# Kernel optimization log

Measured on AMD Instinct MI355X. Metric: run time of the kernel, lower is better.

## Reference

```python
import jax, jax.numpy as jnp
import numpy as np

HIDDEN = 1024
N_EXPERTS = 8
TOP_K = 2
INTER = 1408
N_SHARED = 2
SCALE = 1.0  # routed_scaling_factor


def setup_inputs() -> dict:
    key = jax.random.key(0)
    ks = jax.random.split(key, 9)
    s_h = 1.0 / np.sqrt(HIDDEN)
    s_i = 1.0 / np.sqrt(INTER)
    x = jax.random.normal(ks[0], (2, 2048, HIDDEN), dtype=jnp.float32)
    gate_w = jax.random.uniform(ks[1], (N_EXPERTS, HIDDEN), jnp.float32, -s_h, s_h)  # kaiming_uniform-ish
    # routed experts: SwiGLU (gate, up, down), stacked over experts
    wg = jax.random.uniform(ks[2], (N_EXPERTS, HIDDEN, INTER), jnp.float32, -s_h, s_h)
    wu = jax.random.uniform(ks[3], (N_EXPERTS, HIDDEN, INTER), jnp.float32, -s_h, s_h)
    wd = jax.random.uniform(ks[4], (N_EXPERTS, INTER, HIDDEN), jnp.float32, -s_i, s_i)
    # shared experts: one SwiGLU with intermediate = INTER * N_SHARED
    si = INTER * N_SHARED
    s_si = 1.0 / np.sqrt(si)
    swg = jax.random.uniform(ks[5], (HIDDEN, si), jnp.float32, -s_h, s_h)
    swu = jax.random.uniform(ks[6], (HIDDEN, si), jnp.float32, -s_h, s_h)
    swd = jax.random.uniform(ks[7], (si, HIDDEN), jnp.float32, -s_si, s_si)
    return {"x": x, "gate_w": gate_w, "wg": wg, "wu": wu, "wd": wd,
            "swg": swg, "swu": swu, "swd": swd}


def reference(x, gate_w, wg, wu, wd, swg, swu, swd):
    B, S, H = x.shape
    xf = x.reshape(-1, H)                              # [T, H]
    T = xf.shape[0]
    # --- MoEGate (fp32) ---
    logits = xf.astype(jnp.float32) @ gate_w.astype(jnp.float32).T   # [T, E]
    scores = jax.nn.softmax(logits, axis=-1)
    topw, topi = jax.lax.top_k(scores, TOP_K)          # [T, K]
    denom = topw.sum(axis=-1, keepdims=True) + 1e-20   # norm_topk_prob (top_k > 1)
    topw = topw / denom * SCALE
    # dense combine weights [T, E]: zero except at top-k expert slots
    wdense = jnp.zeros((T, N_EXPERTS), jnp.float32).at[
        jnp.arange(T)[:, None], topi].set(topw)
    # --- routed experts (SwiGLU), computed densely per expert and combined ---
    hg = jnp.einsum('th,ehi->eti', xf, wg)             # [E, T, I]
    hu = jnp.einsum('th,ehi->eti', xf, wu)             # [E, T, I]
    eo = jnp.einsum('eti,eih->eth', jax.nn.silu(hg) * hu, wd)   # [E, T, H]
    y = jnp.einsum('te,eth->th', wdense, eo)           # weighted scatter-combine
    # --- shared experts ---
    shared = (jax.nn.silu(xf @ swg) * (xf @ swu)) @ swd
    return (y + shared).reshape(B, S, H)
```

## Files before the change

kernel.cpp:

```cpp
#include <hip/hip_runtime.h>
#include <hip/hip_bf16.h>
#include <math.h>

#define HIDDEN 1024
#define NEXP 8
#define TOPK 2
#define INTER 1408
#define SINTER 2816
#define NTOK 4096
#define NROWS (NTOK * TOPK)
#define NPANEL 10
#define TROWS 16384
#define MAXT 136

typedef unsigned short ushort_t;
typedef __attribute__((ext_vector_type(8))) short short8;
typedef __attribute__((ext_vector_type(4))) float f32x4;

__device__ __forceinline__ ushort_t f2bf(float f) {
    unsigned int b = __float_as_uint(f);
    unsigned int r = (b + 0x7FFFu + ((b >> 16) & 1u)) >> 16;
    return (ushort_t)r;
}
__device__ __forceinline__ float bf2f(ushort_t u) {
    return __uint_as_float(((unsigned int)u) << 16);
}
__device__ __forceinline__ float silu_f(float g) {
    return g * (1.0f / (1.0f + __expf(-g)));
}
__device__ __forceinline__ int imin(int a, int b) { return a < b ? a : b; }

#define GLDS16(gp, lp) __builtin_amdgcn_global_load_lds(                     \
    (const __attribute__((address_space(1))) void*)(gp),                     \
    (__attribute__((address_space(3))) void*)(lp), 16, 0, 0)

__global__ void conv_x(const float* __restrict__ src, ushort_t* __restrict__ dst) {
    int i = (blockIdx.x * 256 + threadIdx.x) * 4;
    float4 v = *reinterpret_cast<const float4*>(&src[i]);
    union { ushort_t h[4]; unsigned long long ll; } p;
    p.h[0] = f2bf(v.x); p.h[1] = f2bf(v.y); p.h[2] = f2bf(v.z); p.h[3] = f2bf(v.w);
    *reinterpret_cast<unsigned long long*>(&dst[i]) = p.ll;
}

__global__ void tconv(const float* __restrict__ src, ushort_t* __restrict__ dst,
                      int R, int C, long sstride, long dstride) {
    src += (size_t)blockIdx.z * sstride;
    dst += (size_t)blockIdx.z * dstride;
    __shared__ float tile[32][33];
    int ct = blockIdx.x * 32, rt = blockIdx.y * 32;
    int tx = threadIdx.x, ty = threadIdx.y;
#pragma unroll
    for (int i = 0; i < 4; i++)
        tile[ty + 8 * i][tx] = src[(size_t)(rt + ty + 8 * i) * C + ct + tx];
    __syncthreads();
#pragma unroll
    for (int i = 0; i < 4; i++)
        dst[(size_t)(ct + ty + 8 * i) * R + rt + tx] = f2bf(tile[tx][ty + 8 * i]);
}

__global__ void gate_kernel(const float* __restrict__ x, const float* __restrict__ gw,
                            int* __restrict__ top_i, float* __restrict__ top_w) {
    int t = blockIdx.x;
    int lane = threadIdx.x;
    const float* xr = x + (size_t)t * HIDDEN;
    float acc[NEXP];
#pragma unroll
    for (int e = 0; e < NEXP; e++) acc[e] = 0.f;
    for (int j = 0; j < HIDDEN / 64; j++) {
        float xv = xr[lane + 64 * j];
#pragma unroll
        for (int e = 0; e < NEXP; e++)
            acc[e] = fmaf(xv, gw[e * HIDDEN + lane + 64 * j], acc[e]);
    }
#pragma unroll
    for (int e = 0; e < NEXP; e++) {
        float v = acc[e];
        for (int off = 32; off > 0; off >>= 1) v += __shfl_xor(v, off, 64);
        acc[e] = v;
    }
    if (lane == 0) {
        float mx = acc[0];
        for (int e = 1; e < NEXP; e++) mx = fmaxf(mx, acc[e]);
        float s[NEXP];
        float sum = 0.f;
        for (int e = 0; e < NEXP; e++) { s[e] = __expf(acc[e] - mx); sum += s[e]; }
        float inv = 1.0f / sum;
        for (int e = 0; e < NEXP; e++) s[e] *= inv;
        int e0 = 0;
        for (int e = 1; e < NEXP; e++) if (s[e] > s[e0]) e0 = e;
        int e1 = -1;
        for (int e = 0; e < NEXP; e++) {
            if (e == e0) continue;
            if (e1 < 0 || s[e] > s[e1]) e1 = e;
        }
        float w0 = s[e0], w1 = s[e1];
        float denom = w0 + w1 + 1e-20f;
        top_i[t * 2 + 0] = e0;
        top_i[t * 2 + 1] = e1;
        top_w[t * 2 + 0] = w0 / denom;
        top_w[t * 2 + 1] = w1 / denom;
    }
}

__global__ void assign_kernel(const int* __restrict__ top_i, int* __restrict__ cnt,
                              int* __restrict__ rnk) {
    int j = blockIdx.x * blockDim.x + threadIdx.x;
    if (j < NROWS) rnk[j] = atomicAdd(&cnt[top_i[j]], 1);
}

__global__ void scan_kernel(const int* __restrict__ cnt, int* __restrict__ offs2,
                            int* __restrict__ cnt2, int* __restrict__ task_pm) {
    if (threadIdx.x == 0) {
        int o = 0;
        for (int e = 0; e < NEXP; e++) { offs2[e] = o; cnt2[e] = cnt[e]; o += cnt[e]; }
        offs2[8] = NROWS;          cnt2[8] = NTOK;
        offs2[9] = NROWS + NTOK;   cnt2[9] = NTOK;
        offs2[10] = TROWS;
        int t = 0;
        for (int e = 0; e < NPANEL; e++)
            for (int m0 = 0; m0 < cnt2[e]; m0 += 128)
                task_pm[t++] = (e << 16) | (m0 >> 7);
        for (; t < MAXT; t++) task_pm[t] = -1;
    }
}

__global__ void fill_kernel(const int* __restrict__ top_i, const float* __restrict__ top_w,
                            const int* __restrict__ rnk, const int* __restrict__ offs2,
                            int* __restrict__ tok_of_row, float* __restrict__ w_of_row,
                            int* __restrict__ inv_row) {
    int j = blockIdx.x * blockDim.x + threadIdx.x;
    if (j < NROWS) {
        int row = offs2[top_i[j]] + rnk[j];
        tok_of_row[row] = j;
        w_of_row[row] = top_w[j];
        inv_row[j] = row;
    }
}

__global__ void fill_shared(int* __restrict__ tok_of_row) {
    int j = blockIdx.x * blockDim.x + threadIdx.x;
    tok_of_row[NROWS + j] = (j & (NTOK - 1)) << 1;
}

__global__ __launch_bounds__(256, 2) void gemm_gu(
    const ushort_t* __restrict__ xb, const ushort_t* __restrict__ WgT,
    const ushort_t* __restrict__ WuT, ushort_t* __restrict__ act,
    const int* __restrict__ tok_of_row, const int* __restrict__ offs2,
    const int* __restrict__ cnt2, const int* __restrict__ task_pm) {
    int T = gridDim.x;
    int orig = blockIdx.x;
    int logical = (orig & 7) * (T >> 3) + (orig >> 3);
    int task = logical % MAXT;
    int nidx = logical / MAXT;
    int tk = task_pm[task];
    if (tk < 0) return;
    int e = tk >> 16;
    int m0 = (tk & 0xffff) << 7;
    int mcnt = cnt2[e];
    int base = offs2[e];
    int n0 = nidx * 128;
    const ushort_t* Bg = WgT + (size_t)e * INTER * HIDDEN;
    const ushort_t* Bu = WuT + (size_t)e * INTER * HIDDEN;

    __shared__ short As[8 * 512];
    __shared__ short Bgs[8 * 512];
    __shared__ short Bus[8 * 512];

    int tid = threadIdx.x;
    int wave = tid >> 6, lane = tid & 63;
    int wr = wave >> 1, wc = wave & 1;
    int lr = lane & 15;
    int kq = (lane >> 4) * 8;

    int r0 = m0 + 32 * wave + lr, r1 = r0 + 16;
    int rr0 = base + imin(r0, mcnt - 1);
    int rr1 = base + imin(r1, mcnt - 1);
    const ushort_t* srcA0 = xb + (size_t)(tok_of_row[rr0] >> 1) * HIDDEN + kq;
    const ushort_t* srcA1 = xb + (size_t)(tok_of_row[rr1] >> 1) * HIDDEN + kq;
    const ushort_t* srcBg0 = Bg + (size_t)(n0 + 32 * wave + lr) * HIDDEN + kq;
    const ushort_t* srcBg1 = srcBg0 + (size_t)16 * HIDDEN;
    const ushort_t* srcBu0 = Bu + (size_t)(n0 + 32 * wave + lr) * HIDDEN + kq;
    const ushort_t* srcBu1 = srcBu0 + (size_t)16 * HIDDEN;

    f32x4 accG[4][4] = {};
    f32x4 accU[4][4] = {};

    for (int k0 = 0; k0 < HIDDEN; k0 += 32) {
        GLDS16(srcA0 + k0, &As[(2 * wave) * 512]);
        GLDS16(srcA1 + k0, &As[(2 * wave + 1) * 512]);
        GLDS16(srcBg0 + k0, &Bgs[(2 * wave) * 512]);
        GLDS16(srcBg1 + k0, &Bgs[(2 * wave + 1) * 512]);
        GLDS16(srcBu0 + k0, &Bus[(2 * wave) * 512]);
        GLDS16(srcBu1 + k0, &Bus[(2 * wave + 1) * 512]);
        __syncthreads();
        short8 a[4], bg[4], bu[4];
#pragma unroll
        for (int mi = 0; mi < 4; mi++)
            a[mi] = *reinterpret_cast<const short8*>(
                &As[(wr * 4 + mi) * 512 + lane * 8]);
#pragma unroll
        for (int ni = 0; ni < 4; ni++) {
            bg[ni] = *reinterpret_cast<const short8*>(
                &Bgs[(wc * 4 + ni) * 512 + lane * 8]);
            bu[ni] = *reinterpret_cast<const short8*>(
                &Bus[(wc * 4 + ni) * 512 + lane * 8]);
        }
#pragma unroll
        for (int mi = 0; mi < 4; mi++)
#pragma unroll
            for (int ni = 0; ni < 4; ni++) {
                accG[mi][ni] = __builtin_amdgcn_mfma_f32_16x16x32_bf16(
                    a[mi], bg[ni], accG[mi][ni], 0, 0, 0);
                accU[mi][ni] = __builtin_amdgcn_mfma_f32_16x16x32_bf16(
                    a[mi], bu[ni], accU[mi][ni], 0, 0, 0);
            }
        __syncthreads();
    }

#pragma unroll
    for (int mi = 0; mi < 4; mi++) {
#pragma unroll
        for (int r = 0; r < 4; r++) {
            int gm = m0 + wr * 64 + mi * 16 + (lane >> 4) * 4 + r;
            if (gm < mcnt) {
#pragma unroll
                for (int ni = 0; ni < 4; ni++) {
                    int col = n0 + wc * 64 + ni * 16 + lr;
                    float g = accG[mi][ni][r], u = accU[mi][ni][r];
                    act[(size_t)(base + gm) * INTER + col] = f2bf(silu_f(g) * u);
                }
            }
        }
    }
}

__global__ __launch_bounds__(256, 2) void gemm_down(
    const ushort_t* __restrict__ act, const ushort_t* __restrict__ WdT,
    ushort_t* __restrict__ part, const int* __restrict__ offs2,
    const int* __restrict__ cnt2, const int* __restrict__ task_pm) {
    int T = gridDim.x;
    int orig = blockIdx.x;
    int logical = (orig & 7) * (T >> 3) + (orig >> 3);
    int task = logical % MAXT;
    int nidx = logical / MAXT;
    int tk = task_pm[task];
    if (tk < 0) return;
    int e = tk >> 16;
    int m0 = (tk & 0xffff) << 7;
    int mcnt = cnt2[e];
    int base = offs2[e];
    int n0 = nidx * 256;
    const ushort_t* Bd = WdT + (size_t)e * HIDDEN * INTER;

    __shared__ short As[8 * 512];
    __shared__ short Bs[16 * 512];

    int tid = threadIdx.x;
    int wave = tid >> 6, lane = tid & 63;
    int wr = wave >> 1, wc = wave & 1;
    int lr = lane & 15;
    int kq = (lane >> 4) * 8;

    const ushort_t* srcA0 = act + (size_t)(base + m0 + 32 * wave + lr) * INTER + kq;
    const ushort_t* srcA1 = srcA0 + (size_t)16 * INTER;
    const ushort_t* srcB0 = Bd + (size_t)(n0 + 64 * wave + lr) * INTER + kq;
    const ushort_t* srcB1 = srcB0 + (size_t)16 * INTER;
    const ushort_t* srcB2 = srcB0 + (size_t)32 * INTER;
    const ushort_t* srcB3 = srcB0 + (size_t)48 * INTER;

    f32x4 acc[4][8] = {};

    for (int k0 = 0; k0 < INTER; k0 += 32) {
        GLDS16(srcA0 + k0, &As[(2 * wave) * 512]);
        GLDS16(srcA1 + k0, &As[(2 * wave + 1) * 512]);
        GLDS16(srcB0 + k0, &Bs[(4 * wave) * 512]);
        GLDS16(srcB1 + k0, &Bs[(4 * wave + 1) * 512]);
        GLDS16(srcB2 + k0, &Bs[(4 * wave + 2) * 512]);
        GLDS16(srcB3 + k0, &Bs[(4 * wave + 3) * 512]);
        __syncthreads();
        short8 a[4], b[8];
#pragma unroll
        for (int mi = 0; mi < 4; mi++)
            a[mi] = *reinterpret_cast<const short8*>(
                &As[(wr * 4 + mi) * 512 + lane * 8]);
#pragma unroll
        for (int ni = 0; ni < 8; ni++)
            b[ni] = *reinterpret_cast<const short8*>(
                &Bs[(wc * 8 + ni) * 512 + lane * 8]);
#pragma unroll
        for (int mi = 0; mi < 4; mi++)
#pragma unroll
            for (int ni = 0; ni < 8; ni++)
                acc[mi][ni] = __builtin_amdgcn_mfma_f32_16x16x32_bf16(
                    a[mi], b[ni], acc[mi][ni], 0, 0, 0);
        __syncthreads();
    }

#pragma unroll
    for (int mi = 0; mi < 4; mi++) {
#pragma unroll
        for (int r = 0; r < 4; r++) {
            int gm = m0 + wr * 64 + mi * 16 + (lane >> 4) * 4 + r;
            if (gm < mcnt) {
#pragma unroll
                for (int ni = 0; ni < 8; ni++) {
                    int col = n0 + wc * 128 + ni * 16 + lr;
                    part[(size_t)(base + gm) * HIDDEN + col] = f2bf(acc[mi][ni][r]);
                }
            }
        }
    }
}

__global__ __launch_bounds__(256) void combine_kernel(
    const ushort_t* __restrict__ part, const int* __restrict__ inv_row,
    const float* __restrict__ w_of_row, float* __restrict__ out) {
    int t = blockIdx.x;
    int c = threadIdx.x * 4;
    int r0 = inv_row[2 * t], r1 = inv_row[2 * t + 1];
    float w0 = w_of_row[r0], w1 = w_of_row[r1];
    ushort4 a0 = *reinterpret_cast<const ushort4*>(&part[(size_t)r0 * HIDDEN + c]);
    ushort4 a1 = *reinterpret_cast<const ushort4*>(&part[(size_t)r1 * HIDDEN + c]);
    ushort4 a2 = *reinterpret_cast<const ushort4*>(&part[((size_t)NROWS + t) * HIDDEN + c]);
    ushort4 a3 = *reinterpret_cast<const ushort4*>(&part[((size_t)NROWS + NTOK + t) * HIDDEN + c]);
    float4 o;
    o.x = w0 * bf2f(a0.x) + w1 * bf2f(a1.x) + bf2f(a2.x) + bf2f(a3.x);
    o.y = w0 * bf2f(a0.y) + w1 * bf2f(a1.y) + bf2f(a2.y) + bf2f(a3.y);
    o.z = w0 * bf2f(a0.z) + w1 * bf2f(a1.z) + bf2f(a2.z) + bf2f(a3.z);
    o.w = w0 * bf2f(a0.w) + w1 * bf2f(a1.w) + bf2f(a2.w) + bf2f(a3.w);
    *reinterpret_cast<float4*>(&out[(size_t)t * HIDDEN + c]) = o;
}

extern "C" void kernel_launch(void* const* d_in, const int* in_sizes, int n_in,
                              void* d_out, int out_size, void* d_ws, size_t ws_size,
                              hipStream_t stream) {
    const float* x   = (const float*)d_in[0];
    const float* gw  = (const float*)d_in[1];
    const float* wg  = (const float*)d_in[2];
    const float* wu  = (const float*)d_in[3];
    const float* wd  = (const float*)d_in[4];
    const float* swg = (const float*)d_in[5];
    const float* swu = (const float*)d_in[6];
    const float* swd = (const float*)d_in[7];
    float* out = (float*)d_out;

    const size_t XB   = (size_t)NTOK * HIDDEN;
    const size_t WPAN = (size_t)NPANEL * INTER * HIDDEN;
    const size_t ACT  = (size_t)TROWS * INTER;
    const size_t PART = (size_t)TROWS * HIDDEN;
    ushort_t* xb   = (ushort_t*)d_ws;
    ushort_t* wgT  = xb + XB;
    ushort_t* wuT  = wgT + WPAN;
    ushort_t* wdT  = wuT + WPAN;
    ushort_t* act  = wdT + WPAN;
    ushort_t* part = act + ACT;
    int* ib = (int*)(part + PART);
    int* top_i      = ib;
    int* rnk        = ib + NROWS;
    int* cnt        = ib + 2 * NROWS;
    int* offs2      = ib + 2 * NROWS + 8;
    int* cnt2       = offs2 + 16;
    int* task_pm    = cnt2 + 16;
    int* tok_of_row = task_pm + MAXT;
    int* inv_row    = tok_of_row + TROWS;
    float* top_w    = (float*)(inv_row + NROWS);
    float* w_of_row = top_w + NROWS;

    conv_x<<<(NTOK * HIDDEN) / (256 * 4), 256, 0, stream>>>(x, xb);
    dim3 tb(32, 8);
    tconv<<<dim3(INTER / 32, HIDDEN / 32, NEXP), tb, 0, stream>>>(
        wg, wgT, HIDDEN, INTER, (long)HIDDEN * INTER, (long)INTER * HIDDEN);
    tconv<<<dim3(INTER / 32, HIDDEN / 32, NEXP), tb, 0, stream>>>(
        wu, wuT, HIDDEN, INTER, (long)HIDDEN * INTER, (long)INTER * HIDDEN);
    tconv<<<dim3(SINTER / 32, HIDDEN / 32, 1), tb, 0, stream>>>(
        swg, wgT + (size_t)8 * INTER * HIDDEN, HIDDEN, SINTER, 0, 0);
    tconv<<<dim3(SINTER / 32, HIDDEN / 32, 1), tb, 0, stream>>>(
        swu, wuT + (size_t)8 * INTER * HIDDEN, HIDDEN, SINTER, 0, 0);
    tconv<<<dim3(HIDDEN / 32, INTER / 32, NEXP), tb, 0, stream>>>(
        wd, wdT, INTER, HIDDEN, (long)INTER * HIDDEN, (long)HIDDEN * INTER);
    tconv<<<dim3(HIDDEN / 32, INTER / 32, 2), tb, 0, stream>>>(
        swd, wdT + (size_t)8 * HIDDEN * INTER, INTER, HIDDEN,
        (long)INTER * HIDDEN, (long)HIDDEN * INTER);

    gate_kernel<<<NTOK, 64, 0, stream>>>(x, gw, top_i, top_w);
    hipMemsetAsync(cnt, 0, 8 * sizeof(int), stream);
    assign_kernel<<<NROWS / 256, 256, 0, stream>>>(top_i, cnt, rnk);
    scan_kernel<<<1, 1, 0, stream>>>(cnt, offs2, cnt2, task_pm);
    fill_kernel<<<NROWS / 256, 256, 0, stream>>>(top_i, top_w, rnk, offs2,
                                                 tok_of_row, w_of_row, inv_row);
    fill_shared<<<NROWS / 256, 256, 0, stream>>>(tok_of_row);

    gemm_gu<<<MAXT * (INTER / 128), 256, 0, stream>>>(
        xb, wgT, wuT, act, tok_of_row, offs2, cnt2, task_pm);
    gemm_down<<<MAXT * (HIDDEN / 256), 256, 0, stream>>>(
        act, wdT, part, offs2, cnt2, task_pm);
    combine_kernel<<<NTOK, 256, 0, stream>>>(part, inv_row, w_of_row, out);
}
```

Measured before the change: 397.0 us.

## Double-buffer LDS tiles in routed expert GEMMs with prefetch two steps ahead

Both routed-expert GEMM kernels (gate/up and down) now keep two LDS buffers and issue the global-to-LDS loads for tile t+2 while the MFMAs for tile t run. Explicit vmcnt and lgkmcnt waits with raw barriers replace the two __syncthreads per iteration. The MFMA block is also wrapped in s_setprio raises. The goal is to hide global load latency behind compute, at the cost of doubled LDS use, which may reduce occupancy, and correctness that now depends on the hand-counted vmcnt value.

```diff
diff --git a/kernel.cpp b/kernel.cpp
--- a/kernel.cpp
+++ b/kernel.cpp
@@ -162,9 +162,9 @@
     const ushort_t* Bg = WgT + (size_t)e * INTER * HIDDEN;
     const ushort_t* Bu = WuT + (size_t)e * INTER * HIDDEN;
 
-    __shared__ short As[8 * 512];
-    __shared__ short Bgs[8 * 512];
-    __shared__ short Bus[8 * 512];
+    __shared__ short As[2 * 8 * 512];
+    __shared__ short Bgs[2 * 8 * 512];
+    __shared__ short Bus[2 * 8 * 512];
 
     int tid = threadIdx.x;
     int wave = tid >> 6, lane = tid & 63;
@@ -185,26 +185,43 @@
     f32x4 accG[4][4] = {};
     f32x4 accU[4][4] = {};
 
-    for (int k0 = 0; k0 < HIDDEN; k0 += 32) {
-        GLDS16(srcA0 + k0, &As[(2 * wave) * 512]);
-        GLDS16(srcA1 + k0, &As[(2 * wave + 1) * 512]);
-        GLDS16(srcBg0 + k0, &Bgs[(2 * wave) * 512]);
-        GLDS16(srcBg1 + k0, &Bgs[(2 * wave + 1) * 512]);
-        GLDS16(srcBu0 + k0, &Bus[(2 * wave) * 512]);
-        GLDS16(srcBu1 + k0, &Bus[(2 * wave + 1) * 512]);
-        __syncthreads();
+#define STAGE_GU(bo, k0)                                                     \
+    do {                                                                     \
+        GLDS16(srcA0 + (k0), &As[(bo) + (2 * wave) * 512]);                  \
+        GLDS16(srcA1 + (k0), &As[(bo) + (2 * wave + 1) * 512]);              \
+        GLDS16(srcBg0 + (k0), &Bgs[(bo) + (2 * wave) * 512]);                \
+        GLDS16(srcBg1 + (k0), &Bgs[(bo) + (2 * wave + 1) * 512]);            \
+        GLDS16(srcBu0 + (k0), &Bus[(bo) + (2 * wave) * 512]);                \
+        GLDS16(srcBu1 + (k0), &Bus[(bo) + (2 * wave + 1) * 512]);            \
+    } while (0)
+
+    STAGE_GU(0, 0);
+    STAGE_GU(4096, 32);
+
+    const int NT = HIDDEN / 32;
+    for (int t = 0; t < NT; t++) {
+        int bo = (t & 1) << 12;
+        if (t < NT - 1) asm volatile("s_waitcnt vmcnt(6)" ::: "memory");
+        else            asm volatile("s_waitcnt vmcnt(0)" ::: "memory");
+        __builtin_amdgcn_sched_barrier(0);
+        __builtin_amdgcn_s_barrier();
         short8 a[4], bg[4], bu[4];
 #pragma unroll
         for (int mi = 0; mi < 4; mi++)
             a[mi] = *reinterpret_cast<const short8*>(
-                &As[(wr * 4 + mi) * 512 + lane * 8]);
+                &As[bo + (wr * 4 + mi) * 512 + lane * 8]);
 #pragma unroll
         for (int ni = 0; ni < 4; ni++) {
             bg[ni] = *reinterpret_cast<const short8*>(
-                &Bgs[(wc * 4 + ni) * 512 + lane * 8]);
+                &Bgs[bo + (wc * 4 + ni) * 512 + lane * 8]);
             bu[ni] = *reinterpret_cast<const short8*>(
-                &Bus[(wc * 4 + ni) * 512 + lane * 8]);
+                &Bus[bo + (wc * 4 + ni) * 512 + lane * 8]);
         }
+        asm volatile("s_waitcnt lgkmcnt(0)" ::: "memory");
+        __builtin_amdgcn_sched_barrier(0);
+        __builtin_amdgcn_s_barrier();
+        if (t + 2 < NT) STAGE_GU(bo, (t + 2) * 32);
+        __builtin_amdgcn_s_setprio(1);
 #pragma unroll
         for (int mi = 0; mi < 4; mi++)
 #pragma unroll
@@ -214,8 +231,9 @@
                 accU[mi][ni] = __builtin_amdgcn_mfma_f32_16x16x32_bf16(
                     a[mi], bu[ni], accU[mi][ni], 0, 0, 0);
             }
-        __syncthreads();
-    }
+        __builtin_amdgcn_s_setprio(0);
+    }
+#undef STAGE_GU
 
 #pragma unroll
     for (int mi = 0; mi < 4; mi++) {
@@ -252,8 +270,8 @@
     int n0 = nidx * 256;
     const ushort_t* Bd = WdT + (size_t)e * HIDDEN * INTER;
 
-    __shared__ short As[8 * 512];
-    __shared__ short Bs[16 * 512];
+    __shared__ short As[2 * 8 * 512];
+    __shared__ short Bs[2 * 16 * 512];
 
     int tid = threadIdx.x;
     int wave = tid >> 6, lane = tid & 63;
@@ -270,31 +288,50 @@
 
     f32x4 acc[4][8] = {};
 
-    for (int k0 = 0; k0 < INTER; k0 += 32) {
-        GLDS16(srcA0 + k0, &As[(2 * wave) * 512]);
-        GLDS16(srcA1 + k0, &As[(2 * wave + 1) * 512]);
-        GLDS16(srcB0 + k0, &Bs[(4 * wave) * 512]);
-        GLDS16(srcB1 + k0, &Bs[(4 * wave + 1) * 512]);
-        GLDS16(srcB2 + k0, &Bs[(4 * wave + 2) * 512]);
-        GLDS16(srcB3 + k0, &Bs[(4 * wave + 3) * 512]);
-        __syncthreads();
+#define STAGE_D(boA, boB, k0)                                                \
+    do {                                                                     \
+        GLDS16(srcA0 + (k0), &As[(boA) + (2 * wave) * 512]);                 \
+        GLDS16(srcA1 + (k0), &As[(boA) + (2 * wave + 1) * 512]);             \
+        GLDS16(srcB0 + (k0), &Bs[(boB) + (4 * wave) * 512]);                 \
+        GLDS16(srcB1 + (k0), &Bs[(boB) + (4 * wave + 1) * 512]);             \
+        GLDS16(srcB2 + (k0), &Bs[(boB) + (4 * wave + 2) * 512]);             \
+        GLDS16(srcB3 + (k0), &Bs[(boB) + (4 * wave + 3) * 512]);             \
+    } while (0)
+
+    STAGE_D(0, 0, 0);
+    STAGE_D(4096, 8192, 32);
+
+    const int NT = INTER / 32;
+    for (int t = 0; t < NT; t++) {
+        int boA = (t & 1) << 12;
+        int boB = (t & 1) << 13;
+        if (t < NT - 1) asm volatile("s_waitcnt vmcnt(6)" ::: "memory");
+        else            asm volatile("s_waitcnt vmcnt(0)" ::: "memory");
+        __builtin_amdgcn_sched_barrier(0);
+        __builtin_amdgcn_s_barrier();
         short8 a[4], b[8];
 #pragma unroll
         for (int mi = 0; mi < 4; mi++)
             a[mi] = *reinterpret_cast<const short8*>(
-                &As[(wr * 4 + mi) * 512 + lane * 8]);
+                &As[boA + (wr * 4 + mi) * 512 + lane * 8]);
 #pragma unroll
         for (int ni = 0; ni < 8; ni++)
             b[ni] = *reinterpret_cast<const short8*>(
-                &Bs[(wc * 8 + ni) * 512 + lane * 8]);
+                &Bs[boB + (wc * 8 + ni) * 512 + lane * 8]);
+        asm volatile("s_waitcnt lgkmcnt(0)" ::: "memory");
+        __builtin_amdgcn_sched_barrier(0);
+        __builtin_amdgcn_s_barrier();
+        if (t + 2 < NT) STAGE_D(boA, boB, (t + 2) * 32);
+        __builtin_amdgcn_s_setprio(1);
 #pragma unroll
         for (int mi = 0; mi < 4; mi++)
 #pragma unroll
             for (int ni = 0; ni < 8; ni++)
                 acc[mi][ni] = __builtin_amdgcn_mfma_f32_16x16x32_bf16(
                     a[mi], b[ni], acc[mi][ni], 0, 0, 0);
-        __syncthreads();
-    }
+        __builtin_amdgcn_s_setprio(0);
+    }
+#undef STAGE_D
 
 #pragma unroll
     for (int mi = 0; mi < 4; mi++) {
```

Result: faster. 383.7 us, median of 2 (-3.4%).
